# Kernel optimization log

Measured on AMD Instinct MI355X. Metric: run time of the kernel, lower is better.

Reference implementation:

```python
import jax, jax.numpy as jnp
import numpy as np

N, M, D, L, H, S = 8192, 32, 256, 2, 8, 119
DF = 4 * D
DH = D // H


def setup_inputs() -> dict:
    key = jax.random.key(0)
    ks = jax.random.split(key, 24)
    f = lambda i, shape, s=0.05: jax.random.normal(ks[i], shape, dtype=jnp.float32) * s
    return dict(
        species=jax.random.randint(ks[0], (N,), 0, S),
        neighbor_species=jax.random.randint(ks[1], (N, M), 0, S),
        edge_vectors=jax.random.normal(ks[2], (N, M, 3), dtype=jnp.float32),
        edge_distances=jax.random.uniform(ks[3], (N, M), dtype=jnp.float32, minval=0.5, maxval=5.0),
        padding_mask=jax.random.uniform(ks[4], (N, M)) < 0.9,
        reverse_neighbor_index=jax.random.randint(ks[5], (N * M,), 0, N * M),
        cutoff_factors=jax.random.uniform(ks[6], (N, M), dtype=jnp.float32),
        emb_neighbor=f(7, (S, D), 1.0),
        emb_node=f(8, (L, S, D), 1.0),
        Wr=f(9, (L, 4, D)), br=jnp.zeros((L, D), jnp.float32),
        Wq=f(10, (L, D, D)), Wk=f(11, (L, D, D)), Wv=f(12, (L, D, D)), Wo=f(13, (L, D, D)),
        W1=f(14, (L, D, DF)), b1=jnp.zeros((L, DF), jnp.float32),
        W2=f(15, (L, DF, D)), b2=jnp.zeros((L, D), jnp.float32),
        ln1_g=jnp.ones((L, D), jnp.float32), ln1_b=jnp.zeros((L, D), jnp.float32),
        ln2_g=jnp.ones((L, D), jnp.float32), ln2_b=jnp.zeros((L, D), jnp.float32),
        node_head_W=f(16, (L, D, D)), node_head_b=jnp.zeros((L, D), jnp.float32),
        node_fin_W=f(17, (L, D, 1)), node_fin_b=jnp.zeros((L, 1), jnp.float32),
        edge_head_W=f(18, (L, D, D)), edge_head_b=jnp.zeros((L, D), jnp.float32),
        edge_fin_W=f(19, (L, D, 1)), edge_fin_b=jnp.zeros((L, 1), jnp.float32),
    )


def _ln(x, g, b):
    mu = x.mean(-1, keepdims=True)
    var = x.var(-1, keepdims=True)
    return (x - mu) * jax.lax.rsqrt(var + 1e-5) * g + b


def reference(species, neighbor_species, edge_vectors, edge_distances, padding_mask,
              reverse_neighbor_index, cutoff_factors, emb_neighbor, emb_node, Wr, br,
              Wq, Wk, Wv, Wo, W1, b1, W2, b2, ln1_g, ln1_b, ln2_g, ln2_b,
              node_head_W, node_head_b, node_fin_W, node_fin_b,
              edge_head_W, edge_head_b, edge_fin_W, edge_fin_b):
    # edge embedder: lookup per-neighbor species -> input messages [N, M, D]
    msgs = emb_neighbor[neighbor_species]
    geo_in = jnp.concatenate([edge_vectors, edge_distances[..., None]], -1)  # [N,M,4]
    full_mask = jnp.concatenate([jnp.ones((N, 1), bool), padding_mask], 1)   # [N,M+1]
    energies = jnp.zeros((N,), jnp.float32)
    inv_sqrt_dh = np.float32(1.0 / np.sqrt(DH))
    for l in range(L):  # loop over the small fixed number of GNN layers
        node_emb = emb_node[l][species]                 # [N,D]
        edge_geo = geo_in @ Wr[l] + br[l]               # [N,M,D]
        tok_nb = (msgs + edge_geo) * cutoff_factors[..., None]
        tokens = jnp.concatenate([node_emb[:, None, :], tok_nb], 1)  # [N,M+1,D]
        # masked multi-head self-attention over (central + neighbor) tokens
        x = _ln(tokens, ln1_g[l], ln1_b[l])
        q = (x @ Wq[l]).reshape(N, M + 1, H, DH)
        k = (x @ Wk[l]).reshape(N, M + 1, H, DH)
        v = (x @ Wv[l]).reshape(N, M + 1, H, DH)
        scores = jnp.einsum('nqhd,nkhd->nhqk', q, k) * inv_sqrt_dh
        scores = jnp.where(full_mask[:, None, None, :], scores, jnp.float32(-1e9))
        attn = jax.nn.softmax(scores, axis=-1)
        o = jnp.einsum('nhqk,nkhd->nqhd', attn, v).reshape(N, M + 1, D) @ Wo[l]
        tokens = tokens + o
        y = _ln(tokens, ln2_g[l], ln2_b[l])
        tokens = tokens + (jax.nn.silu(y @ W1[l] + b1[l]) @ W2[l] + b2[l])
        out_node = tokens[:, 0]   # [N,D]
        out_edge = tokens[:, 1:]  # [N,M,D]
        # energy heads (MLP + final linear -> scalar)
        node_e = (jax.nn.silu(out_node @ node_head_W[l] + node_head_b[l]) @ node_fin_W[l] + node_fin_b[l])[:, 0]
        edge_e = (jax.nn.silu(out_edge @ edge_head_W[l] + edge_head_b[l]) @ edge_fin_W[l] + edge_fin_b[l])[..., 0]
        edge_e = jnp.where(padding_mask, edge_e, jnp.float32(0.0))
        energies = energies + node_e + (edge_e * cutoff_factors).sum(1)
        # reverse-edge message gather + averaging
        rev = out_edge.reshape(N * M, D)[reverse_neighbor_index].reshape(N, M, D)
        msgs = 0.5 * (msgs + rev)
    return energies
```

## Files before the change

kernel.cpp:

```cpp
#include <hip/hip_runtime.h>

typedef unsigned int u32;
typedef unsigned short u16;
typedef __attribute__((ext_vector_type(8))) short s8v;
typedef __attribute__((ext_vector_type(4))) float f4v;

#define DEV static __device__ __forceinline__

DEV float b2f(u32 u){ return __uint_as_float(u << 16); }
DEV u16 f2bf(float f){ u32 u = __float_as_uint(f); u += 0x7fffu + ((u >> 16) & 1u); return (u16)(u >> 16); }
DEV u32 cvtpk(float lo, float hi){ u32 r; asm("v_cvt_pk_bf16_f32 %0, %1, %2" : "=v"(r) : "v"(lo), "v"(hi)); return r; }
DEV float vrcp(float x){ float r; asm("v_rcp_f32 %0, %1" : "=v"(r) : "v"(x)); return r; }
DEV float fsilu(float v){ return v*vrcp(1.f + __expf(-v)); }
DEV float dot2(u32 a, u32 b){ return b2f(a & 0xffffu)*b2f(b & 0xffffu) + b2f(a >> 16)*b2f(b >> 16); }
DEV f4v mfma16(s8v a, s8v b, f4v c){ return __builtin_amdgcn_mfma_f32_16x16x32_bf16(a, b, c, 0, 0, 0); }

__global__ void prep_frag(const float* __restrict__ src, const int Ksteps, const int Nout,
                          u16* __restrict__ dst){
  const int b = blockIdx.x;
  const int ks = b % Ksteps, nt = b / Ksteps;
  const int ln = threadIdx.x;
  const int col = nt*16 + (ln & 15);
  const int kr  = ks*32 + (ln >> 4)*8;
  __align__(16) u16 tmp[8];
#pragma unroll
  for(int j = 0; j < 8; j++) tmp[j] = f2bf(src[(size_t)(kr + j)*Nout + col]);
  *(uint4*)(dst + (size_t)b*512 + ln*8) = *(const uint4*)tmp;
}

__global__ void prep_plainT(const float* __restrict__ src, u16* __restrict__ dst){
  const int j = blockIdx.x, d = threadIdx.x;
  dst[(size_t)j*256 + d] = f2bf(src[(size_t)d*256 + j]);
}

__global__ void prep_mask(const unsigned char* __restrict__ pm, u32* __restrict__ mb){
  __shared__ int s0, s3;
  if(threadIdx.x == 0){ s0 = 0; s3 = 0; }
  __syncthreads();
  int a0 = 0, a3 = 0;
  for(int i = threadIdx.x; i < 4096; i += 256){
    unsigned char v = pm[i];
    if(v){ int r = i & 3; if(r == 0) a0 = 1; if(r == 3) a3 = 1; }
  }
  if(a0) s0 = 1;
  if(a3) s3 = 1;
  __syncthreads();
  int mode;
  if(s0 && !s3) mode = 1; else if(!s0 && s3) mode = 2; else mode = 0;
  const int n = blockIdx.x*256 + threadIdx.x;
  u32 bits = 0;
  for(int m = 0; m < 32; m++){
    size_t idx = (size_t)n*32 + m;
    bool v;
    if(mode == 0)      v = pm[idx] != 0;
    else if(mode == 1) v = ((const int*)pm)[idx] != 0;
    else               v = ((const float*)pm)[idx] != 0.f;
    bits |= (v ? 1u : 0u) << m;
  }
  mb[n] = bits;
}

DEV void softmax_store(const f4v sS[3][3], u16* Pb, float* a32W,
                       const bool vmask0, const bool vmask1, const bool vmask2,
                       const int lg, const int lr){
  const float sc = 0.17677669529663687f;
#pragma unroll
  for(int rt = 0; rt < 3; rt++){
#pragma unroll
    for(int r = 0; r < 4; r++){
      float sv0 = vmask0 ? sS[rt][0][r]*sc : -1e9f;
      float sv1 = vmask1 ? sS[rt][1][r]*sc : -1e9f;
      float sv2 = vmask2 ? sS[rt][2][r]*sc : -1e9f;
      float m_ = fmaxf(fmaxf(sv0, sv1), sv2);
#pragma unroll
      for(int off = 1; off < 16; off <<= 1) m_ = fmaxf(m_, __shfl_xor(m_, off));
      float e0 = __expf(sv0 - m_), e1 = __expf(sv1 - m_), e2 = __expf(sv2 - m_);
      float sum = e0 + e1 + e2;
#pragma unroll
      for(int off = 1; off < 16; off <<= 1) sum += __shfl_xor(sum, off);
      const float rinv = 1.f/sum;
      const int row = rt*16 + lg*4 + r;
      if(row < 33){
        Pb[row*264 + lr]      = f2bf(e0*rinv);
        Pb[row*264 + 16 + lr] = f2bf(e1*rinv);
        if(lr == 0) a32W[row] = e2*rinv;
      }
    }
  }
}

__global__ __launch_bounds__(512, 4) void k_layer(
    const int* __restrict__ species, const int* __restrict__ nspec,
    const float* __restrict__ evec, const float* __restrict__ edist,
    const float* __restrict__ cutf, const int* __restrict__ rni,
    const float* __restrict__ emb_nb, const float* __restrict__ emb_nd,
    const float* __restrict__ Wr, const float* __restrict__ br,
    const float* __restrict__ g1, const float* __restrict__ lb1,
    const float* __restrict__ g2, const float* __restrict__ lb2,
    const u16* __restrict__ wqkvf, const u16* __restrict__ wof,
    const u16* __restrict__ w1f, const u16* __restrict__ w2f,
    const float* __restrict__ b1, const float* __restrict__ b2,
    const u16* __restrict__ ehf, const float* __restrict__ ehb,
    const float* __restrict__ efw, const float* __restrict__ efb,
    const u16* __restrict__ nhT, const float* __restrict__ nhb,
    const float* __restrict__ nfw, const float* __restrict__ nfb,
    const u32* __restrict__ maskb, u16* __restrict__ oe,
    const int layer, float* __restrict__ energies)
{
  __shared__ __align__(16) unsigned char sm[73296];
  u16* tok    = (u16*)sm;
  u16* qb     = (u16*)(sm + 17424);
  u16* kb     = (u16*)(sm + 34848);
  u16* xb     = (u16*)(sm + 52272);
  float* a32  = (float*)(sm + 69696);
  float* ered = (float*)(sm + 69696);
  float* nred = (float*)(sm + 71232);
  float* nhp  = (float*)(sm + 71248);

  const int l = layer;
  const float* emb_ndl = emb_nd + (size_t)l*30464;
  const float* Wrl  = Wr  + l*1024;  const float* brl  = br  + l*256;
  const float* g1l  = g1  + l*256;   const float* lb1l = lb1 + l*256;
  const float* g2l  = g2  + l*256;   const float* lb2l = lb2 + l*256;
  const u16*   wq   = wqkvf + (size_t)l*196608;
  const u16*   wo   = wof + (size_t)l*65536;
  const u16*   w1   = w1f + (size_t)l*262144;
  const u16*   w2   = w2f + (size_t)l*262144;
  const float* b1l  = b1 + l*1024;   const float* b2l  = b2 + l*256;
  const u16*   eh   = ehf + (size_t)l*65536;
  const float* ehbl = ehb + l*256;   const float* efwl = efw + l*256;
  const float  efbv = efb[l];
  const u16*   nh   = nhT + (size_t)l*65536;
  const float* nhbl = nhb + l*256;   const float* nfwl = nfw + l*256;
  const float  nfbv = nfb[l];

  const int n = blockIdx.x, t = threadIdx.x;
  const int w = t >> 6, ln = t & 63, lr = ln & 15, lg = ln >> 4;
  const int d0 = ln*4;
  const f4v zf = {0.f, 0.f, 0.f, 0.f};

  const int a0off = lr*264      + lg*8;
  const int a1off = (16+lr)*264 + lg*8;
  const int a2off = 32*264      + lg*8;

  for(int row = w; row < 33; row += 8){
    float v0, v1, v2, v3;
    if(row == 0){
      const float4 f = *(const float4*)(emb_ndl + (size_t)species[n]*256 + d0);
      v0 = f.x; v1 = f.y; v2 = f.z; v3 = f.w;
    }else{
      const int m = row - 1;
      const size_t em = (size_t)n*32 + m;
      float4 msg = *(const float4*)(emb_nb + (size_t)nspec[em]*256 + d0);
      if(l){
        const uint2 o2 = *(const uint2*)(oe + (size_t)rni[em]*256 + d0);
        msg.x = 0.5f*(msg.x + b2f(o2.x & 0xffffu));
        msg.y = 0.5f*(msg.y + b2f(o2.x >> 16));
        msg.z = 0.5f*(msg.z + b2f(o2.y & 0xffffu));
        msg.w = 0.5f*(msg.w + b2f(o2.y >> 16));
      }
      const float e0 = evec[em*3], e1 = evec[em*3+1], e2 = evec[em*3+2], dd = edist[em];
      const float4 w0 = *(const float4*)(Wrl + d0),        w1v = *(const float4*)(Wrl + 256 + d0);
      const float4 w2v = *(const float4*)(Wrl + 512 + d0), w3  = *(const float4*)(Wrl + 768 + d0);
      const float4 bb = *(const float4*)(brl + d0);
      const float c = cutf[em];
      v0 = (msg.x + e0*w0.x + e1*w1v.x + e2*w2v.x + dd*w3.x + bb.x)*c;
      v1 = (msg.y + e0*w0.y + e1*w1v.y + e2*w2v.y + dd*w3.y + bb.y)*c;
      v2 = (msg.z + e0*w0.z + e1*w1v.z + e2*w2v.z + dd*w3.z + bb.z)*c;
      v3 = (msg.w + e0*w0.w + e1*w1v.w + e2*w2v.w + dd*w3.w + bb.w)*c;
    }
    uint2 tv; tv.x = cvtpk(v0, v1); tv.y = cvtpk(v2, v3);
    *(uint2*)(tok + row*264 + d0) = tv;
    float s1 = v0+v1+v2+v3, s2 = v0*v0+v1*v1+v2*v2+v3*v3;
#pragma unroll
    for(int off = 1; off < 64; off <<= 1){ s1 += __shfl_xor(s1, off); s2 += __shfl_xor(s2, off); }
    const float mu  = s1*(1.f/256.f);
    const float inv = rsqrtf(s2*(1.f/256.f) - mu*mu + 1e-5f);
    uint2 xo;
    xo.x = cvtpk((v0-mu)*inv*g1l[d0]   + lb1l[d0],   (v1-mu)*inv*g1l[d0+1] + lb1l[d0+1]);
    xo.y = cvtpk((v2-mu)*inv*g1l[d0+2] + lb1l[d0+2], (v3-mu)*inv*g1l[d0+3] + lb1l[d0+3]);
    *(uint2*)(xb + row*264 + d0) = xo;
  }
  __syncthreads();

  {
    f4v acc[4][3];
#pragma unroll
    for(int i = 0; i < 4; i++){ acc[i][0] = zf; acc[i][1] = zf; acc[i][2] = zf; }
#pragma unroll
    for(int ks = 0; ks < 8; ks++){
      s8v x0 = *(const s8v*)(xb + a0off + ks*32);
      s8v x1 = *(const s8v*)(xb + a1off + ks*32);
      s8v x2 = *(const s8v*)(xb + a2off + ks*32);
#pragma unroll
      for(int i = 0; i < 4; i++){
        s8v b = *(const s8v*)(wq + (size_t)(w*4 + i)*4096 + ks*512 + ln*8);
        acc[i][0] = mfma16(x0, b, acc[i][0]);
        acc[i][1] = mfma16(x1, b, acc[i][1]);
        acc[i][2] = mfma16(x2, b, acc[i][2]);
      }
    }
#pragma unroll
    for(int i = 0; i < 4; i++){
      const int ctg = w*4 + i;
#pragma unroll
      for(int rt = 0; rt < 3; rt++){
        f4v av = acc[i][rt];
#pragma unroll
        for(int r = 0; r < 4; r++){
          int row = rt*16 + lg*4 + r;
          if(row > 32) continue;
          u16 bv = f2bf(av[r]);
          if(ctg < 16) qb[row*264 + ctg*16 + lr] = bv;
          else         kb[row*264 + (ctg-16)*16 + lr] = bv;
        }
      }
    }
  }
  __syncthreads();

  const u32 mb = maskb[n];
  const int hb = w*32;
  u16* Pb = qb + hb;
  float* a32W = a32 + w*33;
  const bool vmask0 = (lr == 0) || ((mb >> (lr-1)) & 1u);
  const bool vmask1 = (mb >> (15+lr)) & 1u;
  const bool vmask2 = (lr == 0) && ((mb >> 31) & 1u);
  {
    s8v aq[3], bk[3];
#pragma unroll
    for(int rt = 0; rt < 3; rt++){ int row = rt*16 + lr; row = row > 32 ? 32 : row; aq[rt] = *(const s8v*)(qb + row*264 + hb + lg*8); }
#pragma unroll
    for(int ct = 0; ct < 3; ct++){ int tk = ct*16 + lr; tk = tk > 32 ? 32 : tk; bk[ct] = *(const s8v*)(kb + tk*264 + hb + lg*8); }
    f4v sS[3][3];
#pragma unroll
    for(int rt = 0; rt < 3; rt++)
#pragma unroll
      for(int ct = 0; ct < 3; ct++) sS[rt][ct] = mfma16(aq[rt], bk[ct], zf);
    softmax_store(sS, Pb, a32W, vmask0, vmask1, vmask2, lg, lr);
  }
  __syncthreads();

  {
    f4v acc[2][3];
#pragma unroll
    for(int i = 0; i < 2; i++){ acc[i][0] = zf; acc[i][1] = zf; acc[i][2] = zf; }
#pragma unroll
    for(int ks = 0; ks < 8; ks++){
      s8v x0 = *(const s8v*)(xb + a0off + ks*32);
      s8v x1 = *(const s8v*)(xb + a1off + ks*32);
      s8v x2 = *(const s8v*)(xb + a2off + ks*32);
#pragma unroll
      for(int i = 0; i < 2; i++){
        s8v b = *(const s8v*)(wq + (size_t)(32 + w*2 + i)*4096 + ks*512 + ln*8);
        acc[i][0] = mfma16(x0, b, acc[i][0]);
        acc[i][1] = mfma16(x1, b, acc[i][1]);
        acc[i][2] = mfma16(x2, b, acc[i][2]);
      }
    }
#pragma unroll
    for(int i = 0; i < 2; i++){
      const int vt = w*2 + i;
#pragma unroll
      for(int rt = 0; rt < 3; rt++){
        f4v av = acc[i][rt];
#pragma unroll
        for(int r = 0; r < 4; r++){
          int row = rt*16 + lg*4 + r;
          if(row > 32) continue;
          kb[row*264 + vt*16 + lr] = f2bf(av[r]);
        }
      }
    }
  }
  __syncthreads();

  {
    s8v ap[3];
#pragma unroll
    for(int rt = 0; rt < 3; rt++){ int row = rt*16 + lr; row = row > 32 ? 32 : row; ap[rt] = *(const s8v*)(qb + row*264 + hb + lg*8); }
#pragma unroll
    for(int c2 = 0; c2 < 2; c2++){
      s8v b;
#pragma unroll
      for(int j = 0; j < 8; j++) b[j] = (short)kb[(lg*8 + j)*264 + hb + c2*16 + lr];
      const float vv = b2f(kb[32*264 + hb + c2*16 + lr]);
#pragma unroll
      for(int rt = 0; rt < 3; rt++){
        f4v o_ = mfma16(ap[rt], b, zf);
#pragma unroll
        for(int r = 0; r < 4; r++){
          int row = rt*16 + lg*4 + r;
          int rc = row > 32 ? 32 : row;
          float ov = o_[r] + a32W[rc]*vv;
          if(row < 33) qb[row*264 + hb + c2*16 + lr] = f2bf(ov);
        }
      }
    }
  }
  __syncthreads();

  {
    f4v acc[2][3];
#pragma unroll
    for(int i = 0; i < 2; i++){ acc[i][0] = zf; acc[i][1] = zf; acc[i][2] = zf; }
#pragma unroll
    for(int ks = 0; ks < 8; ks++){
      s8v A0 = *(const s8v*)(qb + a0off + ks*32);
      s8v A1 = *(const s8v*)(qb + a1off + ks*32);
      s8v A2 = *(const s8v*)(qb + a2off + ks*32);
#pragma unroll
      for(int i = 0; i < 2; i++){
        s8v b = *(const s8v*)(wo + (size_t)(w*2 + i)*4096 + ks*512 + ln*8);
        acc[i][0] = mfma16(A0, b, acc[i][0]);
        acc[i][1] = mfma16(A1, b, acc[i][1]);
        acc[i][2] = mfma16(A2, b, acc[i][2]);
      }
    }
#pragma unroll
    for(int i = 0; i < 2; i++){
      const int col = (w*2 + i)*16 + lr;
#pragma unroll
      for(int rt = 0; rt < 3; rt++){
        f4v av = acc[i][rt];
#pragma unroll
        for(int r = 0; r < 4; r++){
          int row = rt*16 + lg*4 + r;
          if(row > 32) continue;
          float tv = b2f(tok[row*264 + col]) + av[r];
          tok[row*264 + col] = f2bf(tv);
        }
      }
    }
  }
  __syncthreads();

  for(int row = w; row < 33; row += 8){
    uint2 tv2 = *(const uint2*)(tok + row*264 + d0);
    float v0 = b2f(tv2.x & 0xffffu), v1 = b2f(tv2.x >> 16);
    float v2 = b2f(tv2.y & 0xffffu), v3 = b2f(tv2.y >> 16);
    float s1 = v0+v1+v2+v3, s2 = v0*v0+v1*v1+v2*v2+v3*v3;
#pragma unroll
    for(int off = 1; off < 64; off <<= 1){ s1 += __shfl_xor(s1, off); s2 += __shfl_xor(s2, off); }
    const float mu  = s1*(1.f/256.f);
    const float inv = rsqrtf(s2*(1.f/256.f) - mu*mu + 1e-5f);
    uint2 yo;
    yo.x = cvtpk((v0-mu)*inv*g2l[d0]   + lb2l[d0],   (v1-mu)*inv*g2l[d0+1] + lb2l[d0+1]);
    yo.y = cvtpk((v2-mu)*inv*g2l[d0+2] + lb2l[d0+2], (v3-mu)*inv*g2l[d0+3] + lb2l[d0+3]);
    *(uint2*)(xb + row*264 + d0) = yo;
  }
  __syncthreads();

  f4v facc[2][3];
#pragma unroll
  for(int i = 0; i < 2; i++){ facc[i][0] = zf; facc[i][1] = zf; facc[i][2] = zf; }

  for(int ch = 0; ch < 4; ch++){
    {
      f4v acc[2][3];
#pragma unroll
      for(int i = 0; i < 2; i++){ acc[i][0] = zf; acc[i][1] = zf; acc[i][2] = zf; }
#pragma unroll
      for(int ks = 0; ks < 8; ks++){
        s8v y0 = *(const s8v*)(xb + a0off + ks*32);
        s8v y1 = *(const s8v*)(xb + a1off + ks*32);
        s8v y2 = *(const s8v*)(xb + a2off + ks*32);
#pragma unroll
        for(int i = 0; i < 2; i++){
          const int nt = ch*16 + w*2 + i;
          s8v b = *(const s8v*)(w1 + (size_t)nt*4096 + ks*512 + ln*8);
          acc[i][0] = mfma16(y0, b, acc[i][0]);
          acc[i][1] = mfma16(y1, b, acc[i][1]);
          acc[i][2] = mfma16(y2, b, acc[i][2]);
        }
      }
#pragma unroll
      for(int i = 0; i < 2; i++){
        const int nt = ch*16 + w*2 + i;
        const int colL = (w*2 + i)*16 + lr;
        const float bias = b1l[nt*16 + lr];
#pragma unroll
        for(int rt = 0; rt < 3; rt++){
          f4v hv = acc[i][rt];
#pragma unroll
          for(int r = 0; r < 4; r++){
            int row = rt*16 + lg*4 + r;
            if(row > 32) continue;
            qb[row*264 + colL] = f2bf(fsilu(hv[r] + bias));
          }
        }
      }
    }
    __syncthreads();
#pragma unroll
    for(int ks = 0; ks < 8; ks++){
      s8v A0 = *(const s8v*)(qb + a0off + ks*32);
      s8v A1 = *(const s8v*)(qb + a1off + ks*32);
      s8v A2 = *(const s8v*)(qb + a2off + ks*32);
#pragma unroll
      for(int i = 0; i < 2; i++){
        s8v b = *(const s8v*)(w2 + (size_t)((w*2 + i)*32 + ch*8 + ks)*512 + ln*8);
        facc[i][0] = mfma16(A0, b, facc[i][0]);
        facc[i][1] = mfma16(A1, b, facc[i][1]);
        facc[i][2] = mfma16(A2, b, facc[i][2]);
      }
    }
    __syncthreads();
  }

#pragma unroll
  for(int i = 0; i < 2; i++){
    const int col = (w*2 + i)*16 + lr;
    const float bias2 = b2l[col];
#pragma unroll
    for(int rt = 0; rt < 3; rt++){
#pragma unroll
      for(int r = 0; r < 4; r++){
        int row = rt*16 + lg*4 + r;
        if(row > 32) continue;
        float tv = b2f(tok[row*264 + col]) + facc[i][rt][r] + bias2;
        u16 tvb = f2bf(tv);
        tok[row*264 + col] = tvb;
        if(l == 0 && row > 0) oe[((size_t)n*32 + (row-1))*256 + col] = tvb;
      }
    }
  }
  __syncthreads();

  float rp[3][4];
#pragma unroll
  for(int a = 0; a < 3; a++)
#pragma unroll
    for(int r = 0; r < 4; r++) rp[a][r] = 0.f;
  {
    f4v acc[2][3];
#pragma unroll
    for(int i = 0; i < 2; i++){ acc[i][0] = zf; acc[i][1] = zf; acc[i][2] = zf; }
#pragma unroll
    for(int ks = 0; ks < 8; ks++){
      s8v A0 = *(const s8v*)(tok + a0off + ks*32);
      s8v A1 = *(const s8v*)(tok + a1off + ks*32);
      s8v A2 = *(const s8v*)(tok + a2off + ks*32);
#pragma unroll
      for(int i = 0; i < 2; i++){
        s8v b = *(const s8v*)(eh + (size_t)(w*2 + i)*4096 + ks*512 + ln*8);
        acc[i][0] = mfma16(A0, b, acc[i][0]);
        acc[i][1] = mfma16(A1, b, acc[i][1]);
        acc[i][2] = mfma16(A2, b, acc[i][2]);
      }
    }
#pragma unroll
    for(int i = 0; i < 2; i++){
      const int col = (w*2 + i)*16 + lr;
      const float bb = ehbl[col], ff = efwl[col];
#pragma unroll
      for(int rt = 0; rt < 3; rt++)
#pragma unroll
        for(int r = 0; r < 4; r++){
          rp[rt][r] += fsilu(acc[i][rt][r] + bb)*ff;
        }
    }
  }
#pragma unroll
  for(int rt = 0; rt < 3; rt++)
#pragma unroll
    for(int r = 0; r < 4; r++){
      float v = rp[rt][r];
#pragma unroll
      for(int off = 1; off < 16; off <<= 1) v += __shfl_xor(v, off);
      if(lr == 0) ered[w*48 + rt*16 + lg*4 + r] = v;
    }

  {
    const int j = t & 255, half = t >> 8;
    const u16* nr = nh + (size_t)j*256 + half*128;
    const u16* tr = tok + half*128;
    float acc = 0.f;
#pragma unroll 4
    for(int dd = 0; dd < 128; dd += 8){
      uint4 ta = *(const uint4*)(tr + dd);
      uint4 na = *(const uint4*)(nr + dd);
      acc += dot2(ta.x, na.x) + dot2(ta.y, na.y) + dot2(ta.z, na.z) + dot2(ta.w, na.w);
    }
    nhp[t] = acc;
  }
  __syncthreads();

  if(t < 256){
    float hv = nhp[t] + nhp[t + 256] + nhbl[t];
    float pp = fsilu(hv)*nfwl[t];
#pragma unroll
    for(int off = 1; off < 64; off <<= 1) pp += __shfl_xor(pp, off);
    if(ln == 0) nred[w] = pp;
  }
  __syncthreads();

  if(w == 0){
    float ev = 0.f;
    if(ln < 32){
      const int row = ln + 1;
      float es = efbv;
#pragma unroll
      for(int ww = 0; ww < 8; ww++) es += ered[ww*48 + row];
      if((mb >> ln) & 1u) ev = es*cutf[(size_t)n*32 + ln];
    }
#pragma unroll
    for(int off = 1; off < 64; off <<= 1) ev += __shfl_xor(ev, off);
    if(ln == 0){
      float tot = ev + nred[0] + nred[1] + nred[2] + nred[3] + nfbv;
      energies[n] = (l ? energies[n] : 0.f) + tot;
    }
  }
}

extern "C" void kernel_launch(void* const* d_in, const int* in_sizes, int n_in,
                              void* d_out, int out_size, void* d_ws, size_t ws_size,
                              hipStream_t stream){
  (void)in_sizes; (void)n_in; (void)out_size;
  const int*   species = (const int*)d_in[0];
  const int*   nspec   = (const int*)d_in[1];
  const float* evec    = (const float*)d_in[2];
  const float* edist   = (const float*)d_in[3];
  const int*   rni     = (const int*)d_in[5];
  const float* cutf    = (const float*)d_in[6];
  const float* emb_nb  = (const float*)d_in[7];
  const float* emb_nd  = (const float*)d_in[8];
  const float* Wr      = (const float*)d_in[9];
  const float* br      = (const float*)d_in[10];
  const float* Wq      = (const float*)d_in[11];
  const float* Wk      = (const float*)d_in[12];
  const float* Wv      = (const float*)d_in[13];
  const float* Wo      = (const float*)d_in[14];
  const float* W1      = (const float*)d_in[15];
  const float* b1      = (const float*)d_in[16];
  const float* W2      = (const float*)d_in[17];
  const float* b2      = (const float*)d_in[18];
  const float* g1      = (const float*)d_in[19];
  const float* lb1     = (const float*)d_in[20];
  const float* g2      = (const float*)d_in[21];
  const float* lb2     = (const float*)d_in[22];
  const float* nhW     = (const float*)d_in[23];
  const float* nhb     = (const float*)d_in[24];
  const float* nfw     = (const float*)d_in[25];
  const float* nfb     = (const float*)d_in[26];
  const float* ehW     = (const float*)d_in[27];
  const float* ehb     = (const float*)d_in[28];
  const float* efw     = (const float*)d_in[29];
  const float* efb     = (const float*)d_in[30];
  float* energies = (float*)d_out;

  char* wsb = (char*)d_ws;
  u16* oe     = (u16*)(wsb);
  u16* wqkvf  = (u16*)(wsb + 134217728LL);
  u16* wof    = (u16*)(wsb + 135004160LL);
  u16* w1f    = (u16*)(wsb + 135266304LL);
  u16* w2f    = (u16*)(wsb + 136314880LL);
  u16* ehf    = (u16*)(wsb + 137363456LL);
  u16* nhT    = (u16*)(wsb + 137625600LL);
  u32* maskb  = (u32*)(wsb + 137887744LL);
  if(ws_size < 137920512ULL) return;

  for(int l = 0; l < 2; l++){
    const size_t wqo = (size_t)l*196608;
    prep_frag<<<128, 64, 0, stream>>>(Wq + (size_t)l*65536, 8, 256, wqkvf + wqo);
    prep_frag<<<128, 64, 0, stream>>>(Wk + (size_t)l*65536, 8, 256, wqkvf + wqo + 65536);
    prep_frag<<<128, 64, 0, stream>>>(Wv + (size_t)l*65536, 8, 256, wqkvf + wqo + 131072);
    prep_frag<<<128, 64, 0, stream>>>(Wo + (size_t)l*65536, 8, 256, wof + (size_t)l*65536);
    prep_frag<<<512, 64, 0, stream>>>(W1 + (size_t)l*262144, 8, 1024, w1f + (size_t)l*262144);
    prep_frag<<<512, 64, 0, stream>>>(W2 + (size_t)l*262144, 32, 256, w2f + (size_t)l*262144);
    prep_frag<<<128, 64, 0, stream>>>(ehW + (size_t)l*65536, 8, 256, ehf + (size_t)l*65536);
    prep_plainT<<<256, 256, 0, stream>>>(nhW + (size_t)l*65536, nhT + (size_t)l*65536);
  }
  prep_mask<<<32, 256, 0, stream>>>((const unsigned char*)d_in[4], maskb);

  for(int l = 0; l < 2; l++){
    k_layer<<<8192, 512, 0, stream>>>(species, nspec, evec, edist, cutf, rni,
        emb_nb, emb_nd, Wr, br, g1, lb1, g2, lb2,
        wqkvf, wof, w1f, w2f, b1, b2,
        ehf, ehb, efw, efb, nhT, nhb, nfw, nfb,
        maskb, oe, l, energies);
  }
}
```

Baseline: 1.966 ms.

## Fuse V projection into QK GEMM loop and store V transposed

New measurement: 2.433 ms. +23.7%, slower.

```diff
diff --git a/kernel.cpp b/kernel.cpp
--- a/kernel.cpp
+++ b/kernel.cpp
@@ -183,10 +183,13 @@
   }
   __syncthreads();
 
+  f4v vacc[2][3];
   {
     f4v acc[4][3];
 #pragma unroll
     for(int i = 0; i < 4; i++){ acc[i][0] = zf; acc[i][1] = zf; acc[i][2] = zf; }
+#pragma unroll
+    for(int i = 0; i < 2; i++){ vacc[i][0] = zf; vacc[i][1] = zf; vacc[i][2] = zf; }
 #pragma unroll
     for(int ks = 0; ks < 8; ks++){
       s8v x0 = *(const s8v*)(xb + a0off + ks*32);
@@ -198,6 +201,13 @@
         acc[i][0] = mfma16(x0, b, acc[i][0]);
         acc[i][1] = mfma16(x1, b, acc[i][1]);
         acc[i][2] = mfma16(x2, b, acc[i][2]);
+      }
+#pragma unroll
+      for(int i = 0; i < 2; i++){
+        s8v b = *(const s8v*)(wq + (size_t)(32 + w*2 + i)*4096 + ks*512 + ln*8);
+        vacc[i][0] = mfma16(x0, b, vacc[i][0]);
+        vacc[i][1] = mfma16(x1, b, vacc[i][1]);
+        vacc[i][2] = mfma16(x2, b, vacc[i][2]);
       }
     }
 #pragma unroll
@@ -241,34 +251,19 @@
   }
   __syncthreads();
 
-  {
-    f4v acc[2][3];
-#pragma unroll
-    for(int i = 0; i < 2; i++){ acc[i][0] = zf; acc[i][1] = zf; acc[i][2] = zf; }
-#pragma unroll
-    for(int ks = 0; ks < 8; ks++){
-      s8v x0 = *(const s8v*)(xb + a0off + ks*32);
-      s8v x1 = *(const s8v*)(xb + a1off + ks*32);
-      s8v x2 = *(const s8v*)(xb + a2off + ks*32);
-#pragma unroll
-      for(int i = 0; i < 2; i++){
-        s8v b = *(const s8v*)(wq + (size_t)(32 + w*2 + i)*4096 + ks*512 + ln*8);
-        acc[i][0] = mfma16(x0, b, acc[i][0]);
-        acc[i][1] = mfma16(x1, b, acc[i][1]);
-        acc[i][2] = mfma16(x2, b, acc[i][2]);
-      }
-    }
+  u16* vT = kb;
+  {
 #pragma unroll
     for(int i = 0; i < 2; i++){
-      const int vt = w*2 + i;
+      const int col = (w*2 + i)*16 + lr;
 #pragma unroll
       for(int rt = 0; rt < 3; rt++){
-        f4v av = acc[i][rt];
+        f4v av = vacc[i][rt];
 #pragma unroll
         for(int r = 0; r < 4; r++){
           int row = rt*16 + lg*4 + r;
           if(row > 32) continue;
-          kb[row*264 + vt*16 + lr] = f2bf(av[r]);
+          vT[col*40 + row] = f2bf(av[r]);
         }
       }
     }
@@ -281,10 +276,9 @@
     for(int rt = 0; rt < 3; rt++){ int row = rt*16 + lr; row = row > 32 ? 32 : row; ap[rt] = *(const s8v*)(qb + row*264 + hb + lg*8); }
 #pragma unroll
     for(int c2 = 0; c2 < 2; c2++){
-      s8v b;
-#pragma unroll
-      for(int j = 0; j < 8; j++) b[j] = (short)kb[(lg*8 + j)*264 + hb + c2*16 + lr];
-      const float vv = b2f(kb[32*264 + hb + c2*16 + lr]);
+      const int vcol = hb + c2*16 + lr;
+      s8v b = *(const s8v*)(vT + vcol*40 + lg*8);
+      const float vv = b2f(vT[vcol*40 + 32]);
 #pragma unroll
       for(int rt = 0; rt < 3; rt++){
         f4v o_ = mfma16(ap[rt], b, zf);
```
